# Performance work log

Measured on AMD Instinct MI355X. Metric: run time of the kernel, lower is better.

The kernel has to match this reference:

```python
import jax, jax.numpy as jnp
import numpy as np

DN = ('NCHW', 'OIHW', 'NCHW')

def conv(x, w, b, stride=1, pad=1):
    y = jax.lax.conv_general_dilated(x, w, (stride, stride), [(pad, pad), (pad, pad)], dimension_numbers=DN)
    return y + b[None, :, None, None]

def conv_t(x, w, b):
    # torch ConvTranspose2d(k=4, s=2, p=1): implemented as lhs-dilated conv, pad = k-1-p = 2
    y = jax.lax.conv_general_dilated(x, w, (1, 1), [(2, 2), (2, 2)], lhs_dilation=(2, 2), dimension_numbers=DN)
    return y + b[None, :, None, None]

def residual_stack(x, rw3, rb3, rw1, rb1):
    # canonical VQ-VAE residual block: x + conv1x1(relu(conv3x3(relu(x)))), then final relu
    n = rw3.shape[0]
    for i in range(n):
        h = conv(jax.nn.relu(x), rw3[i], rb3[i], 1, 1)
        h = conv(jax.nn.relu(h), rw1[i], rb1[i], 1, 0)
        x = x + h
    return jax.nn.relu(x)

def vq(x, codebook, beta):
    # x: [N, D, H, W] -> [N, H, W, D]
    x = jnp.transpose(x, (0, 2, 3, 1))
    shp = x.shape
    xf = x.reshape(-1, shp[-1])                               # [T, D]
    d = (jnp.sum(xf * xf, 1, keepdims=True)
         + jnp.sum(codebook * codebook, 1)
         - 2.0 * xf @ codebook.T)                             # [T, K]
    idx = jnp.argmin(d, axis=1)                               # [T]
    enc = jax.nn.one_hot(idx, codebook.shape[0], dtype=x.dtype)
    q = jnp.take(codebook, idx, axis=0).reshape(shp)
    loss_e = jnp.mean((jax.lax.stop_gradient(q) - x) ** 2)
    loss_q = jnp.mean((q - jax.lax.stop_gradient(x)) ** 2)
    loss = loss_q + beta * loss_e
    q_st = x + jax.lax.stop_gradient(q - x)
    p = jnp.mean(enc, axis=0)
    perplexity = jnp.exp(-jnp.sum(p * jnp.log(p + 1e-10)))
    return loss, jnp.transpose(q_st, (0, 3, 1, 2)), perplexity, enc

def setup_inputs() -> dict:
    key = jax.random.key(0)
    ks = jax.random.split(key, 24)
    C_img, C, RH, NR, K, D = 3, 128, 32, 2, 512, 64
    def g(k, shape, fan_in):
        return jax.random.normal(k, shape, jnp.float32) * (1.0 / np.sqrt(fan_in))
    inp = {
        'x': jax.random.normal(ks[0], (16, C_img, 256, 256), jnp.float32),
        'enc_w1': g(ks[1], (C // 2, C_img, 4, 4), C_img * 16), 'enc_b1': jnp.zeros((C // 2,)),
        'enc_w2': g(ks[2], (C, C // 2, 4, 4), C // 2 * 16), 'enc_b2': jnp.zeros((C,)),
        'enc_w3': g(ks[3], (C, C, 3, 3), C * 9), 'enc_b3': jnp.zeros((C,)),
        'enc_rw3': g(ks[4], (NR, RH, C, 3, 3), C * 9), 'enc_rb3': jnp.zeros((NR, RH)),
        'enc_rw1': g(ks[5], (NR, C, RH, 1, 1), RH), 'enc_rb1': jnp.zeros((NR, C)),
        'pre_w': g(ks[6], (D, C, 1, 1), C), 'pre_b': jnp.zeros((D,)),
        'codebook': jax.random.uniform(ks[7], (K, D), jnp.float32, -1.0 / K, 1.0 / K),
        'dec_w1': g(ks[8], (C, D, 3, 3), D * 9), 'dec_b1': jnp.zeros((C,)),
        'dec_rw3': g(ks[9], (NR, RH, C, 3, 3), C * 9), 'dec_rb3': jnp.zeros((NR, RH)),
        'dec_rw1': g(ks[10], (NR, C, RH, 1, 1), RH), 'dec_rb1': jnp.zeros((NR, C)),
        'dec_dw1': g(ks[11], (C // 2, C, 4, 4), C * 16), 'dec_db1': jnp.zeros((C // 2,)),
        'dec_dw2': g(ks[12], (C_img, C // 2, 4, 4), C // 2 * 16), 'dec_db2': jnp.zeros((C_img,)),
    }
    return inp

def reference(x, enc_w1, enc_b1, enc_w2, enc_b2, enc_w3, enc_b3, enc_rw3, enc_rb3, enc_rw1, enc_rb1,
              pre_w, pre_b, codebook, dec_w1, dec_b1, dec_rw3, dec_rb3, dec_rw1, dec_rb1,
              dec_dw1, dec_db1, dec_dw2, dec_db2):
    beta = 0.25
    # encoder
    h = jax.nn.relu(conv(x, enc_w1, enc_b1, 2, 1))
    h = jax.nn.relu(conv(h, enc_w2, enc_b2, 2, 1))
    h = conv(h, enc_w3, enc_b3, 1, 1)
    h = residual_stack(h, enc_rw3, enc_rb3, enc_rw1, enc_rb1)
    # pre-VQ 1x1 conv
    z = conv(h, pre_w, pre_b, 1, 0)
    # vector quantization
    loss, q, perplexity, _ = vq(z, codebook, beta)
    # decoder
    d = conv(q, dec_w1, dec_b1, 1, 1)
    d = residual_stack(d, dec_rw3, dec_rb3, dec_rw1, dec_rb1)
    d = jax.nn.relu(conv_t(d, dec_dw1, dec_db1))
    x_recon = conv_t(d, dec_dw2, dec_db2)
    return loss, x_recon, perplexity
```

## Files before the change

### kernel.cpp

```cpp
#include <hip/hip_runtime.h>

typedef __attribute__((ext_vector_type(8)))  short bf16x8;
typedef __attribute__((ext_vector_type(16))) float f32x16;
typedef unsigned long long u64t;

__device__ __forceinline__ int swzu(int u)
{
    return u ^ (((u >> 3) & 1) | (((u >> 4) & 1) << 1));
}

__device__ __forceinline__ void fsplit(float v, unsigned short& h, unsigned short& l)
{
    union { float f; unsigned u; } a; a.f = v;
    unsigned uh = a.u + 0x7fffu + ((a.u >> 16) & 1u);
    h = (unsigned short)(uh >> 16);
    union { float f; unsigned u; } hb; hb.u = (unsigned)h << 16;
    float r = v - hb.f;
    union { float f; unsigned u; } b; b.f = r;
    unsigned ul = b.u + 0x7fffu + ((b.u >> 16) & 1u);
    l = (unsigned short)(ul >> 16);
}

__device__ __forceinline__ float bf2f(unsigned short u)
{
    union { float f; unsigned v; } a; a.v = (unsigned)u << 16; return a.f;
}

__global__ void pack_w(const float* __restrict__ w, unsigned short* __restrict__ hi,
                       unsigned short* __restrict__ lo, int Cout, int Cin, int KK,
                       int CoP, int CiP)
{
    int i = blockIdx.x * 256 + threadIdx.x;
    int tot = KK * CoP * CiP;
    if (i >= tot) return;
    int t  = i / (CoP * CiP);
    int r  = i - t * (CoP * CiP);
    int co = r / CiP;
    int ci = r - co * CiP;
    float v = (co < Cout && ci < Cin) ? w[((size_t)co * Cin + ci) * KK + t] : 0.f;
    unsigned short h, l;
    fsplit(v, h, l);
    hi[i] = h; lo[i] = l;
}

__global__ void cb_norm(const float* __restrict__ cb, float* __restrict__ cn)
{
    int i = blockIdx.x * 256 + threadIdx.x;
    if (i >= 512) return;
    float s = 0.f;
    for (int d = 0; d < 64; d++) s = fmaf(cb[i*64+d], cb[i*64+d], s);
    cn[i] = s;
}

__global__ __launch_bounds__(256) void pack_x(const float* __restrict__ x,
    unsigned short* __restrict__ PH)
{
    int idx = blockIdx.x * 256 + threadIdx.x;
    int n = idx >> 16, pix = idx & 65535;
    unsigned short h[8], l[8];
#pragma unroll
    for (int c = 0; c < 8; c++) h[c] = 0;
#pragma unroll
    for (int c = 0; c < 3; c++) {
        float v = x[((size_t)(n * 3 + c) << 16) + pix];
        fsplit(v, h[c], l[c]);
    }
    uint4 hv;
    hv.x = h[0] | ((unsigned)h[1] << 16); hv.y = h[2] | ((unsigned)h[3] << 16);
    hv.z = h[4] | ((unsigned)h[5] << 16); hv.w = h[6] | ((unsigned)h[7] << 16);
    uint4 z4 = make_uint4(0, 0, 0, 0);
    size_t b0 = (((size_t)(n * 2) << 16) + pix) * 8;
    size_t b1 = (((size_t)(n * 2 + 1) << 16) + pix) * 8;
    *(uint4*)(PH + b0) = hv;
    *(uint4*)(PH + b1) = z4;
}

template<int K,int S,int P,int CIP,int COUT,int HIN,int WIN,int HOUT,int WOUT,
         int TR,int TC,int WM,int WN,int PX2,int CO2,int CC,int CO_PAD,
         bool PACK,bool PRELU,bool PLO,bool WF32,bool ROUT,bool RES>
__global__ __launch_bounds__(256) void conv_mfma(
    const unsigned short* __restrict__ inH,
    const unsigned short* __restrict__ wpH,
    const float* __restrict__ bias, const float* __restrict__ res,
    float* __restrict__ outF, unsigned short* __restrict__ outPH,
    unsigned short* __restrict__ outPL)
{
    constexpr int IHT = (TR - 1) * S + K;
    constexpr int IW  = (TC - 1) * S + K;
    constexpr int PS  = IHT * IW;
    constexpr int PLN = CC * 2;
    constexpr int UN  = PS * PLN;
    constexpr int KK  = K * K;
    constexpr int NCH = CIP / (CC * 16);
    constexpr int NBUF = (NCH > 1) ? 2 : 1;
    constexpr int CG  = CIP / 8;
    constexpr int CGO = (COUT + 7) / 8;
    constexpr int XB  = WOUT / TC;
    constexpr int REGU = (UN + 255) / 256;
    constexpr int NST = CC * KK;

    __shared__ uint4 lbH[NBUF * UN];

    const int tid = threadIdx.x;
    const int bx  = blockIdx.x;
    const int r0  = (bx / XB) * TR;
    const int c0  = (bx % XB) * TC;
    const int co0 = blockIdx.y * (WM * CO2 * 32);
    const int n   = blockIdx.z;

    const int l  = tid & 63, wv = tid >> 6;
    const int wm = wv / WN, wn = wv % WN;
    const int ln = l & 31, kg = l >> 5;

    int pb[PX2], gyv[PX2], gxv[PX2];
#pragma unroll
    for (int p2 = 0; p2 < PX2; p2++) {
        int q = wn * (PX2 * 32) + p2 * 32 + ln;
        int lr = q / TC, lc = q % TC;
        pb[p2] = (lr * S) * IW + lc * S;
        gyv[p2] = r0 + lr; gxv[p2] = c0 + lc;
    }

    const int iy0 = r0 * S - P, ix0 = c0 * S - P;
    const size_t inb = (size_t)n * CG * HIN * WIN;

    f32x16 acc[PX2][CO2];
#pragma unroll
    for (int p2 = 0; p2 < PX2; p2++)
#pragma unroll
        for (int g = 0; g < CO2; g++) acc[p2][g] = (f32x16){};

    auto unit_load = [&](int u, int cgb, uint4& hv){
        int kgu = u / PS, pos = u - kgu * PS;
        int py = pos / IW, px = pos - py * IW;
        int gy = iy0 + py, gx = ix0 + px;
        bool ok = ((unsigned)gy < (unsigned)HIN) && ((unsigned)gx < (unsigned)WIN);
        hv = make_uint4(0,0,0,0);
        if (ok) {
            size_t a = (inb + ((size_t)(cgb + kgu) * HIN + gy) * WIN + gx) * 8;
            hv = *(const uint4*)(inH + a);
        }
    };

    auto stage_direct = [&](int kc, int b){
        for (int idx = tid; idx < UN; idx += 256) {
            uint4 hv;
            unit_load(idx, kc * PLN, hv);
            lbH[b * UN + swzu(idx)] = hv;
        }
    };

    uint4 rvH[REGU];
    auto load_regs = [&](int kc){
#pragma unroll
        for (int rr = 0; rr < REGU; rr++) {
            int idx = tid + rr * 256;
            uint4 hv = make_uint4(0,0,0,0);
            if (idx < UN) unit_load(idx, kc * PLN, hv);
            rvH[rr] = hv;
        }
    };
    auto write_regs = [&](int b){
#pragma unroll
        for (int rr = 0; rr < REGU; rr++) {
            int idx = tid + rr * 256;
            if (idx < UN) lbH[b * UN + swzu(idx)] = rvH[rr];
        }
    };

    auto compute = [&](int kc, int b){
        bf16x8 aR[4][CO2], bR[3][PX2];
        auto loadA = [&](int step, bf16x8 (&a)[CO2]){
            const int ks = step / KK, t = step - ks * KK;
#pragma unroll
            for (int g = 0; g < CO2; g++) {
                const int coA = co0 + (wm * CO2 + g) * 32 + ln;
                const size_t wo = ((size_t)t * CO_PAD + coA) * CIP
                                + kc * (CC * 16) + ks * 16 + kg * 8;
                a[g] = *(const bf16x8*)(wpH + wo);
            }
        };
        auto loadB = [&](int step, bf16x8 (&bv)[PX2]){
            const int ks = step / KK, t = step - ks * KK;
            const int ky = t / K, kx = t - ky * K;
#pragma unroll
            for (int p2 = 0; p2 < PX2; p2++) {
                const int u = (ks * 2 + kg) * PS + pb[p2] + ky * IW + kx;
                bv[p2] = *(const bf16x8*)&lbH[b * UN + swzu(u)];
            }
        };
        loadA(0, aR[0]);
        if (NST > 1) loadA(1, aR[1]);
        if (NST > 2) loadA(2, aR[2]);
        loadB(0, bR[0]);
        if (NST > 1) loadB(1, bR[1]);
        __builtin_amdgcn_s_setprio(1);
#pragma unroll
        for (int step = 0; step < NST; step++) {
            if (step + 3 < NST) loadA(step + 3, aR[(step + 3) & 3]);
            if (step + 2 < NST) loadB(step + 2, bR[(step + 2) % 3]);
#pragma unroll
            for (int p2 = 0; p2 < PX2; p2++)
#pragma unroll
                for (int g = 0; g < CO2; g++)
                    acc[p2][g] = __builtin_amdgcn_mfma_f32_32x32x16_bf16(
                        aR[step & 3][g], bR[step % 3][p2], acc[p2][g], 0, 0, 0);
        }
        __builtin_amdgcn_s_setprio(0);
    };

    stage_direct(0, 0);
    __syncthreads();
    int cur = 0;
    for (int kc = 0; kc < NCH; kc++) {
        const bool more = (kc + 1 < NCH);
        if (more) load_regs(kc + 1);
        compute(kc, cur);
        if (more) {
            write_regs(cur ^ 1);
            __syncthreads();
            cur ^= 1;
        }
    }

    const size_t HWo = (size_t)HOUT * WOUT;
#pragma unroll
    for (int p2 = 0; p2 < PX2; p2++) {
        const int gy = gyv[p2], gx = gxv[p2];
#pragma unroll
        for (int g = 0; g < CO2; g++) {
            const int co32 = co0 + (wm * CO2 + g) * 32;
#pragma unroll
            for (int rq = 0; rq < 4; rq++) {
                const int cb4 = co32 + 8 * rq + 4 * kg;
                float v[4];
#pragma unroll
                for (int i = 0; i < 4; i++) {
                    const int r = rq * 4 + i;
                    const int co = cb4 + i;
                    float bv = (co < COUT) ? bias[co] : 0.f;
                    float vv = acc[p2][g][r] + bv;
                    if (RES && co < COUT)
                        vv += res[((size_t)n * COUT + co) * HWo + (size_t)gy * WOUT + gx];
                    if (ROUT) vv = fmaxf(vv, 0.f);
                    if (WF32 && co < COUT)
                        outF[((size_t)n * COUT + co) * HWo + (size_t)gy * WOUT + gx] = vv;
                    v[i] = vv;
                }
                if (PACK) {
                    u64t uh = 0, ul = 0;
#pragma unroll
                    for (int i = 0; i < 4; i++) {
                        float pv = PRELU ? fmaxf(v[i], 0.f) : v[i];
                        unsigned short ph, pl;
                        fsplit(pv, ph, pl);
                        uh |= (u64t)ph << (16 * i);
                        ul |= (u64t)pl << (16 * i);
                    }
                    size_t pa = (((size_t)n * CGO + (co32 >> 3) + rq) * HOUT + gy) * (size_t)WOUT * 8
                              + (size_t)gx * 8 + 4 * kg;
                    *(u64t*)(outPH + pa) = uh;
                    if (PLO) *(u64t*)(outPL + pa) = ul;
                }
            }
        }
    }
}

template<int CIP,int COUT,int HW,int CO_PAD,
         bool PACK,bool PRELU,bool PLO,bool WF32,bool ROUT,bool RES>
__global__ __launch_bounds__(256) void conv1x1_mfma(
    const unsigned short* __restrict__ inH,
    const unsigned short* __restrict__ wpH,
    const float* __restrict__ bias, const float* __restrict__ res,
    float* __restrict__ outF, unsigned short* __restrict__ outPH,
    unsigned short* __restrict__ outPL)
{
    constexpr int NCH = CIP / 16;
    constexpr int CG  = CIP / 8;
    constexpr int CGO = (COUT + 7) / 8;

    const int tid = threadIdx.x;
    const int bx  = blockIdx.x;
    const int co0 = blockIdx.y * 64;
    const int n   = blockIdx.z;

    const int l  = tid & 63, wv = tid >> 6;
    const int wm = wv >> 1, wn = wv & 1;
    const int ln = l & 31, kg = l >> 5;

    const int pix = bx * 64 + wn * 32 + ln;
    const int coA = co0 + wm * 32 + ln;

    f32x16 acc = {};
#pragma unroll
    for (int kc = 0; kc < NCH; kc++) {
        bf16x8 b = *(const bf16x8*)(inH + ((size_t)(n * CG + kc * 2 + kg) * HW + pix) * 8);
        bf16x8 a = *(const bf16x8*)(wpH + ((size_t)coA * CIP + kc * 16 + kg * 8));
        acc = __builtin_amdgcn_mfma_f32_32x32x16_bf16(a, b, acc, 0, 0, 0);
    }

    const int co32 = co0 + wm * 32;
#pragma unroll
    for (int rq = 0; rq < 4; rq++) {
        const int cb4 = co32 + 8 * rq + 4 * kg;
        float v[4];
#pragma unroll
        for (int i = 0; i < 4; i++) {
            const int r = rq * 4 + i;
            const int co = cb4 + i;
            float bv = (co < COUT) ? bias[co] : 0.f;
            float vv = acc[r] + bv;
            if (RES && co < COUT)
                vv += res[((size_t)n * COUT + co) * HW + pix];
            if (ROUT) vv = fmaxf(vv, 0.f);
            if (WF32 && co < COUT)
                outF[((size_t)n * COUT + co) * HW + pix] = vv;
            v[i] = vv;
        }
        if (PACK) {
            u64t uh = 0, ul = 0;
#pragma unroll
            for (int i = 0; i < 4; i++) {
                float pv = PRELU ? fmaxf(v[i], 0.f) : v[i];
                unsigned short ph, pl;
                fsplit(pv, ph, pl);
                uh |= (u64t)ph << (16 * i);
                ul |= (u64t)pl << (16 * i);
            }
            size_t pa = (((size_t)n * CGO + (co32 >> 3) + rq) * HW + pix) * 8 + 4 * kg;
            *(u64t*)(outPH + pa) = uh;
            if (PLO) *(u64t*)(outPL + pa) = ul;
        }
    }
}

template<int CIP,int COUT,int HIN,int WIN,int CO2,int CC,int CO_PAD,
         bool PACK,bool WF32,bool ROUT>
__global__ __launch_bounds__(256) void convt_mfma(
    const unsigned short* __restrict__ inH,
    const unsigned short* __restrict__ wpH,
    const float* __restrict__ bias, float* __restrict__ outF,
    unsigned short* __restrict__ outPH)
{
    constexpr int HOUT = 2 * HIN, WOUT = 2 * WIN;
    constexpr int XHN  = WOUT / 128;
    constexpr int PS   = 3 * 68;
    constexpr int PLN  = CC * 2;
    constexpr int UN   = PS * PLN;
    constexpr int NCH  = CIP / (CC * 16);
    constexpr int NBUF = (NCH > 1) ? 2 : 1;
    constexpr int CG   = CIP / 8;
    constexpr int CGO  = (COUT + 7) / 8;
    constexpr int REGU = (UN + 255) / 256;
    constexpr int NST  = CC * 4;

    __shared__ uint4 lbH[NBUF * UN];

    const int tid = threadIdx.x;
    const int xh  = blockIdx.x % XHN;
    const int gr  = blockIdx.x / XHN;
    const int oy0 = (gr >> 1) * 4 + (gr & 1);
    const int co0 = blockIdx.y * (CO2 * 32);
    const int n   = blockIdx.z;

    const int ky0 = oy0 & 1;
    const int iyb = ((oy0 + ky0) >> 1) - 1;

    const int l  = tid & 63, wv = tid >> 6;
    const int pw = wv & 1, xb = wv >> 1;
    const int ln = l & 31, kg = l >> 5;

    const size_t inb = (size_t)n * CG * HIN * WIN;

    f32x16 acc[2][CO2];
#pragma unroll
    for (int r2 = 0; r2 < 2; r2++)
#pragma unroll
        for (int g = 0; g < CO2; g++) acc[r2][g] = (f32x16){};

    auto unit_load = [&](int u, int cgb, uint4& hv){
        int kgu = u / PS, pos = u - kgu * PS;
        int rr = pos / 68, cc = pos - rr * 68;
        int gy = iyb + rr, gx = xh * 64 + cc - 1;
        bool ok = ((unsigned)gy < (unsigned)HIN) && ((unsigned)gx < (unsigned)WIN);
        hv = make_uint4(0,0,0,0);
        if (ok) {
            size_t a = (inb + ((size_t)(cgb + kgu) * HIN + gy) * WIN + gx) * 8;
            hv = *(const uint4*)(inH + a);
        }
    };

    auto stage_direct = [&](int kc, int b){
        for (int idx = tid; idx < UN; idx += 256) {
            uint4 hv;
            unit_load(idx, kc * PLN, hv);
            lbH[b * UN + swzu(idx)] = hv;
        }
    };

    uint4 rvH[REGU];
    auto load_regs = [&](int kc){
#pragma unroll
        for (int rr = 0; rr < REGU; rr++) {
            int idx = tid + rr * 256;
            uint4 hv = make_uint4(0,0,0,0);
            if (idx < UN) unit_load(idx, kc * PLN, hv);
            rvH[rr] = hv;
        }
    };
    auto write_regs = [&](int b){
#pragma unroll
        for (int rr = 0; rr < REGU; rr++) {
            int idx = tid + rr * 256;
            if (idx < UN) lbH[b * UN + swzu(idx)] = rvH[rr];
        }
    };

    auto compute = [&](int kc, int b){
        bf16x8 aR[4][CO2], bR[3][2];
        auto loadA = [&](int step, bf16x8 (&a)[CO2]){
            const int ks = step / 4, tt = step - ks * 4;
            const int widx = (ky0 + 2 * (tt >> 1)) * 4 + (pw + 2 * (tt & 1));
#pragma unroll
            for (int g = 0; g < CO2; g++) {
                const int coA = co0 + g * 32 + ln;
                const size_t wo = ((size_t)widx * CO_PAD + coA) * CIP
                                + kc * (CC * 16) + ks * 16 + kg * 8;
                a[g] = *(const bf16x8*)(wpH + wo);
            }
        };
        auto loadB = [&](int step, bf16x8 (&bv)[2]){
            const int ks = step / 4, tt = step - ks * 4;
            const int ty = tt >> 1, tx = tt & 1;
#pragma unroll
            for (int r2 = 0; r2 < 2; r2++) {
                const int u = (ks * 2 + kg) * PS + (r2 + ty) * 68 + xb * 32 + ln + pw + tx;
                bv[r2] = *(const bf16x8*)&lbH[b * UN + swzu(u)];
            }
        };
        loadA(0, aR[0]);
        if (NST > 1) loadA(1, aR[1]);
        if (NST > 2) loadA(2, aR[2]);
        loadB(0, bR[0]);
        if (NST > 1) loadB(1, bR[1]);
        __builtin_amdgcn_s_setprio(1);
#pragma unroll
        for (int step = 0; step < NST; step++) {
            if (step + 3 < NST) loadA(step + 3, aR[(step + 3) & 3]);
            if (step + 2 < NST) loadB(step + 2, bR[(step + 2) % 3]);
#pragma unroll
            for (int r2 = 0; r2 < 2; r2++)
#pragma unroll
                for (int g = 0; g < CO2; g++)
                    acc[r2][g] = __builtin_amdgcn_mfma_f32_32x32x16_bf16(
                        aR[step & 3][g], bR[step % 3][r2], acc[r2][g], 0, 0, 0);
        }
        __builtin_amdgcn_s_setprio(0);
    };

    stage_direct(0, 0);
    __syncthreads();
    int cur = 0;
    for (int kc = 0; kc < NCH; kc++) {
        const bool more = (kc + 1 < NCH);
        if (more) load_regs(kc + 1);
        compute(kc, cur);
        if (more) {
            write_regs(cur ^ 1);
            __syncthreads();
            cur ^= 1;
        }
    }

    const int ox = xh * 128 + pw + 2 * (xb * 32 + ln);
    const size_t HWo = (size_t)HOUT * WOUT;
#pragma unroll
    for (int r2 = 0; r2 < 2; r2++) {
        const int oy = oy0 + 2 * r2;
#pragma unroll
        for (int g = 0; g < CO2; g++) {
            const int co32 = co0 + g * 32;
#pragma unroll
            for (int rq = 0; rq < 4; rq++) {
                const int cb4 = co32 + 8 * rq + 4 * kg;
                float v[4];
#pragma unroll
                for (int i = 0; i < 4; i++) {
                    const int r = rq * 4 + i;
                    const int co = cb4 + i;
                    float bv = (co < COUT) ? bias[co] : 0.f;
                    float vv = acc[r2][g][r] + bv;
                    if (ROUT) vv = fmaxf(vv, 0.f);
                    if (WF32 && co < COUT)
                        outF[((size_t)n * COUT + co) * HWo + (size_t)oy * WOUT + ox] = vv;
                    v[i] = vv;
                }
                if (PACK) {
                    u64t uh = 0;
#pragma unroll
                    for (int i = 0; i < 4; i++) {
                        unsigned short ph, pl;
                        fsplit(v[i], ph, pl);
                        uh |= (u64t)ph << (16 * i);
                    }
                    size_t pa = (((size_t)n * CGO + (co32 >> 3) + rq) * HOUT + oy) * (size_t)WOUT * 8
                              + (size_t)ox * 8 + 4 * kg;
                    *(u64t*)(outPH + pa) = uh;
                }
            }
        }
    }
}

__global__ __launch_bounds__(256) void vq_mfma(
    const unsigned short* __restrict__ zPH, const unsigned short* __restrict__ zPL,
    const unsigned short* __restrict__ cbH, const unsigned short* __restrict__ cbL,
    const float* __restrict__ cnorm,
    unsigned short* __restrict__ qPH,
    float* __restrict__ ssep, int* __restrict__ hist)
{
    __shared__ unsigned short zH[128 * 72];
    __shared__ unsigned short zL[128 * 72];
    __shared__ float cnl[512];
    __shared__ int   hl[512];

    const int tid = threadIdx.x;
    const int blk = blockIdx.x;

    for (int i = tid; i < 512; i += 256) { cnl[i] = cnorm[i]; hl[i] = 0; }

    for (int idx = tid; idx < 1024; idx += 256) {
        int tok = idx >> 3, cg = idx & 7;
        int t = blk * 128 + tok;
        int n = t >> 12, pix = t & 4095;
        size_t a = (((size_t)(n * 8 + cg)) * 4096 + pix) * 8;
        *(uint4*)&zH[tok * 72 + cg * 8] = *(const uint4*)(zPH + a);
        *(uint4*)&zL[tok * 72 + cg * 8] = *(const uint4*)(zPL + a);
    }
    __syncthreads();

    const int l  = tid & 63, wv = tid >> 6;
    const int ln = l & 31, kg = l >> 5;
    const int tok = wv * 32 + ln;

    float xn = 0.f;
#pragma unroll
    for (int j8 = 0; j8 < 8; j8++) {
        bf16x8 vH = *(const bf16x8*)&zH[tok * 72 + j8 * 8];
        bf16x8 vL = *(const bf16x8*)&zL[tok * 72 + j8 * 8];
#pragma unroll
        for (int j = 0; j < 8; j++) {
            float xv = bf2f((unsigned short)vH[j]) + bf2f((unsigned short)vL[j]);
            xn = fmaf(xv, xv, xn);
        }
    }

    float bm = 3.4e38f; int bidx = 0;
    for (int cg = 0; cg < 16; cg++) {
        f32x16 a0 = {}, a1 = {};
#pragma unroll
        for (int ks = 0; ks < 4; ks++) {
            const size_t wo = ((size_t)(cg * 32 + ln)) * 64 + ks * 16 + kg * 8;
            bf16x8 aH = *(const bf16x8*)(cbH + wo);
            bf16x8 aL = *(const bf16x8*)(cbL + wo);
            bf16x8 bH = *(const bf16x8*)&zH[tok * 72 + ks * 16 + kg * 8];
            bf16x8 bL = *(const bf16x8*)&zL[tok * 72 + ks * 16 + kg * 8];
            a0 = __builtin_amdgcn_mfma_f32_32x32x16_bf16(aH, bH, a0, 0, 0, 0);
            a1 = __builtin_amdgcn_mfma_f32_32x32x16_bf16(aH, bL, a1, 0, 0, 0);
            a1 = __builtin_amdgcn_mfma_f32_32x32x16_bf16(aL, bH, a1, 0, 0, 0);
        }
#pragma unroll
        for (int r = 0; r < 16; r++) {
            int m    = (r & 3) + 8 * (r >> 2) + 4 * kg;
            int code = cg * 32 + m;
            float s  = a0[r] + a1[r];
            float dm = cnl[code] - 2.f * s;
            if (dm < bm) { bm = dm; bidx = code; }
        }
    }

    float bm2 = __shfl_xor(bm, 32);
    int   bi2 = __shfl_xor(bidx, 32);
    if (bm2 < bm || (bm2 == bm && bi2 < bidx)) { bm = bm2; bidx = bi2; }

    {
        int t = blk * 128 + tok;
        int n = t >> 12, pix = t & 4095;
#pragma unroll
        for (int cgl = 0; cgl < 4; cgl++) {
            int cg = kg * 4 + cgl;
            uint4 hv = *(const uint4*)(cbH + (size_t)bidx * 64 + cg * 8);
            size_t a = (((size_t)(n * 8 + cg)) * 4096 + pix) * 8;
            *(uint4*)(qPH + a) = hv;
        }
    }

    float bestd = xn + bm;
    float c = (kg == 0) ? bestd : 0.f;
#pragma unroll
    for (int o = 32; o > 0; o >>= 1) c += __shfl_down(c, o, 64);
    if (l == 0) ssep[blk * 4 + wv] = c;
    if (kg == 0) atomicAdd(&hl[bidx], 1);
    __syncthreads();
    for (int i = tid; i < 512; i += 256) if (hl[i] > 0) atomicAdd(&hist[i], hl[i]);
}

__global__ void vq_init(int* hist)
{
    for (int i = threadIdx.x; i < 512; i += 256) hist[i] = 0;
}

__global__ __launch_bounds__(256) void vq_finalize(
    const float* __restrict__ ssep, const int* __restrict__ hist,
    float* __restrict__ o_loss, float* __restrict__ o_perp)
{
    __shared__ float red[256];
    const int tid = threadIdx.x;
    float h = 0.f;
    for (int i = tid; i < 512; i += 256) {
        float p = (float)hist[i] * (1.0f / 65536.0f);
        h -= p * logf(p + 1e-10f);
    }
    red[tid] = h;
    __syncthreads();
    for (int st = 128; st > 0; st >>= 1) {
        if (tid < st) red[tid] += red[tid + st];
        __syncthreads();
    }
    const float H = red[0];
    __syncthreads();
    float s = 0.f;
    for (int i = tid; i < 2048; i += 256) s += ssep[i];
    red[tid] = s;
    __syncthreads();
    for (int st = 128; st > 0; st >>= 1) {
        if (tid < st) red[tid] += red[tid + st];
        __syncthreads();
    }
    if (tid == 0) {
        *o_loss = 1.25f * red[0] / 4194304.0f;
        *o_perp = expf(H);
    }
}

extern "C" void kernel_launch(void* const* d_in, const int* in_sizes, int n_in,
                              void* d_out, int out_size, void* d_ws, size_t ws_size,
                              hipStream_t stream)
{
    const float* x       = (const float*)d_in[0];
    const float* enc_w1  = (const float*)d_in[1];
    const float* enc_b1  = (const float*)d_in[2];
    const float* enc_w2  = (const float*)d_in[3];
    const float* enc_b2  = (const float*)d_in[4];
    const float* enc_w3  = (const float*)d_in[5];
    const float* enc_b3  = (const float*)d_in[6];
    const float* enc_rw3 = (const float*)d_in[7];
    const float* enc_rb3 = (const float*)d_in[8];
    const float* enc_rw1 = (const float*)d_in[9];
    const float* enc_rb1 = (const float*)d_in[10];
    const float* pre_w   = (const float*)d_in[11];
    const float* pre_b   = (const float*)d_in[12];
    const float* cb      = (const float*)d_in[13];
    const float* dec_w1  = (const float*)d_in[14];
    const float* dec_b1  = (const float*)d_in[15];
    const float* dec_rw3 = (const float*)d_in[16];
    const float* dec_rb3 = (const float*)d_in[17];
    const float* dec_rw1 = (const float*)d_in[18];
    const float* dec_rb1 = (const float*)d_in[19];
    const float* dw1     = (const float*)d_in[20];
    const float* db1     = (const float*)d_in[21];
    const float* dw2     = (const float*)d_in[22];
    const float* db2     = (const float*)d_in[23];

    float* o      = (float*)d_out;
    float* loss_p = o;
    float* recon  = o + 1;
    float* perp_p = o + 1 + 16 * 3 * 256 * 256;

    unsigned short* R1H = (unsigned short*)d_ws;
    unsigned short* R1L = R1H + 16777216;
    unsigned short* R2H = R1L + 16777216;
    unsigned short* R2L = R2H + 16777216;
    float* Cf  = (float*)(R2L + 16777216);
    float* SSE = Cf + 8388608;
    int*   HIST = (int*)(SSE + 2048);

    unsigned short *xPH = R1H;
    unsigned short *BPH = R1H;
    unsigned short *zPH = R1H + 8388608, *zPL = R1L + 8388608;
    unsigned short *DtPH = R1H + 12582912;
    unsigned short *dAPH = R1H;
    unsigned short *APH = R2H;
    unsigned short *CPH = R2H;
    unsigned short *qPH = R2H + 8388608;

    unsigned short* wp_cur = (unsigned short*)(((size_t)(HIST + 512) + 31) & ~(size_t)31);
    auto carve = [&](size_t n_us) {
        unsigned short* p = wp_cur;
        wp_cur += ((n_us + 15) & ~(size_t)15);
        return p;
    };
    auto PK = [&](const float* w, unsigned short* hi, unsigned short* lo,
                  int Co, int Ci, int KK, int CoP, int CiP) {
        int tot = KK * CoP * CiP;
        pack_w<<<dim3((tot + 255) / 256), dim3(256), 0, stream>>>(w, hi, lo, Co, Ci, KK, CoP, CiP);
    };

    unsigned short *e1H = carve(16*64*16),  *e1L = carve(16*64*16);
    unsigned short *e2H = carve(16*128*64), *e2L = carve(16*128*64);
    unsigned short *e3H = carve(9*128*128), *e3L = carve(9*128*128);
    unsigned short *er3aH = carve(9*32*128), *er3aL = carve(9*32*128);
    unsigned short *er3bH = carve(9*32*128), *er3bL = carve(9*32*128);
    unsigned short *er1aH = carve(128*32),   *er1aL = carve(128*32);
    unsigned short *er1bH = carve(128*32),   *er1bL = carve(128*32);
    unsigned short *preH = carve(64*128),    *preL = carve(64*128);
    unsigned short *d1H  = carve(9*128*64),  *d1L  = carve(9*128*64);
    unsigned short *dr3aH = carve(9*32*128), *dr3aL = carve(9*32*128);
    unsigned short *dr3bH = carve(9*32*128), *dr3bL = carve(9*32*128);
    unsigned short *dr1aH = carve(128*32),   *dr1aL = carve(128*32);
    unsigned short *dr1bH = carve(128*32),   *dr1bL = carve(128*32);
    unsigned short *ct1H = carve(16*64*128), *ct1L = carve(16*64*128);
    unsigned short *ct2H = carve(16*32*64),  *ct2L = carve(16*32*64);
    unsigned short *cbH  = carve(512*64),    *cbL  = carve(512*64);
    float* CN = (float*)carve(1024);

    PK(enc_w1, e1H, e1L, 64, 3, 16, 64, 16);
    PK(enc_w2, e2H, e2L, 128, 64, 16, 128, 64);
    PK(enc_w3, e3H, e3L, 128, 128, 9, 128, 128);
    PK(enc_rw3,             er3aH, er3aL, 32, 128, 9, 32, 128);
    PK(enc_rw3 + 32*128*9,  er3bH, er3bL, 32, 128, 9, 32, 128);
    PK(enc_rw1,             er1aH, er1aL, 128, 32, 1, 128, 32);
    PK(enc_rw1 + 128*32,    er1bH, er1bL, 128, 32, 1, 128, 32);
    PK(pre_w, preH, preL, 64, 128, 1, 64, 128);
    PK(dec_w1, d1H, d1L, 128, 64, 9, 128, 64);
    PK(dec_rw3,             dr3aH, dr3aL, 32, 128, 9, 32, 128);
    PK(dec_rw3 + 32*128*9,  dr3bH, dr3bL, 32, 128, 9, 32, 128);
    PK(dec_rw1,             dr1aH, dr1aL, 128, 32, 1, 128, 32);
    PK(dec_rw1 + 128*32,    dr1bH, dr1bL, 128, 32, 1, 128, 32);
    PK(dw1, ct1H, ct1L, 64, 128, 16, 64, 128);
    PK(dw2, ct2H, ct2L, 3, 64, 16, 32, 64);
    PK(cb,  cbH,  cbL,  512, 64, 1, 512, 64);
    cb_norm<<<dim3(2), dim3(256), 0, stream>>>(cb, CN);
    pack_x<<<dim3(4096), dim3(256), 0, stream>>>(x, xPH);

    const int N = 16;

    conv_mfma<4,2,1, 16,64, 256,256, 128,128, 2,64, 2,2,2,1, 1, 64,
              true,false,false,false,true,false>
        <<<dim3(128,1,N),256,0,stream>>>(xPH, e1H, enc_b1, nullptr, nullptr, APH, nullptr);
    conv_mfma<4,2,1, 64,128, 128,128, 64,64, 2,64, 2,2,2,2, 1, 128,
              true,false,false,false,true,false>
        <<<dim3(32,1,N),256,0,stream>>>(APH, e2H, enc_b2, nullptr, nullptr, BPH, nullptr);
    conv_mfma<3,1,1, 128,128, 64,64, 64,64, 2,64, 2,2,2,2, 2, 128,
              true,true,false,true,false,false>
        <<<dim3(32,1,N),256,0,stream>>>(BPH, e3H, enc_b3, nullptr, Cf, CPH, nullptr);
    conv_mfma<3,1,1, 128,32, 64,64, 64,64, 2,64, 1,4,1,1, 2, 32,
              true,true,false,false,false,false>
        <<<dim3(32,1,N),256,0,stream>>>(CPH, er3aH, enc_rb3, nullptr, nullptr, DtPH, nullptr);
    conv1x1_mfma<32,128, 4096, 128,  true,true,false,true,false,true>
        <<<dim3(64,2,N),256,0,stream>>>(DtPH, er1aH, enc_rb1, Cf, Cf, CPH, nullptr);
    conv_mfma<3,1,1, 128,32, 64,64, 64,64, 2,64, 1,4,1,1, 2, 32,
              true,true,false,false,false,false>
        <<<dim3(32,1,N),256,0,stream>>>(CPH, er3bH, enc_rb3 + 32, nullptr, nullptr, DtPH, nullptr);
    conv1x1_mfma<32,128, 4096, 128,  true,true,false,true,false,true>
        <<<dim3(64,2,N),256,0,stream>>>(DtPH, er1bH, enc_rb1 + 128, Cf, Cf, CPH, nullptr);
    conv1x1_mfma<128,64, 4096, 64,   true,false,true,false,false,false>
        <<<dim3(64,1,N),256,0,stream>>>(CPH, preH, pre_b, nullptr, nullptr, zPH, zPL);

    vq_init<<<dim3(1), dim3(256), 0, stream>>>(HIST);
    vq_mfma<<<dim3(512), dim3(256), 0, stream>>>(zPH, zPL, cbH, cbL, CN, qPH, SSE, HIST);
    vq_finalize<<<dim3(1), dim3(256), 0, stream>>>(SSE, HIST, loss_p, perp_p);

    conv_mfma<3,1,1, 64,128, 64,64, 64,64, 2,64, 2,2,2,2, 2, 128,
              true,true,false,true,false,false>
        <<<dim3(32,1,N),256,0,stream>>>(qPH, d1H, dec_b1, nullptr, Cf, CPH, nullptr);
    conv_mfma<3,1,1, 128,32, 64,64, 64,64, 2,64, 1,4,1,1, 2, 32,
              true,true,false,false,false,false>
        <<<dim3(32,1,N),256,0,stream>>>(CPH, dr3aH, dec_rb3, nullptr, nullptr, DtPH, nullptr);
    conv1x1_mfma<32,128, 4096, 128,  true,true,false,true,false,true>
        <<<dim3(64,2,N),256,0,stream>>>(DtPH, dr1aH, dec_rb1, Cf, Cf, CPH, nullptr);
    conv_mfma<3,1,1, 128,32, 64,64, 64,64, 2,64, 1,4,1,1, 2, 32,
              true,true,false,false,false,false>
        <<<dim3(32,1,N),256,0,stream>>>(CPH, dr3bH, dec_rb3 + 32, nullptr, nullptr, DtPH, nullptr);
    conv1x1_mfma<32,128, 4096, 128,  true,true,false,true,false,true>
        <<<dim3(64,2,N),256,0,stream>>>(DtPH, dr1bH, dec_rb1 + 128, Cf, Cf, CPH, nullptr);
    convt_mfma<128,64, 64,64, 2, 2, 64,  true,false,true>
        <<<dim3(64,1,N),256,0,stream>>>(CPH, ct1H, db1, nullptr, dAPH);
    convt_mfma<64,3, 128,128, 1, 2, 32,  false,true,false>
        <<<dim3(256,1,N),256,0,stream>>>(dAPH, ct2H, db2, recon, nullptr);
}
```

Measured before the change: 533.6 us.

## Preload all A-fragments per chunk and split output channels across grid y

The conv and transposed-conv compute loops now load every weight fragment for the whole K-chunk into registers up front, replacing the rolling 4-deep prefetch ring. Three 128-output-channel convs drop one CO2 template parameter from 2 to 1 and double grid.y, so each block covers half the output channels. Together these cut per-thread register pressure from accumulators and double the number of blocks in flight. In exchange the input tile staged in shared memory is now loaded twice, once per channel half, and the larger upfront weight array may raise VGPR use for the larger NST shapes.

```diff
diff --git a/kernel.cpp b/kernel.cpp
--- a/kernel.cpp
+++ b/kernel.cpp
@@ -169,17 +169,19 @@
     };
 
     auto compute = [&](int kc, int b){
-        bf16x8 aR[4][CO2], bR[3][PX2];
-        auto loadA = [&](int step, bf16x8 (&a)[CO2]){
-            const int ks = step / KK, t = step - ks * KK;
+        bf16x8 aF[NST * CO2];
+#pragma unroll
+        for (int s2 = 0; s2 < NST; s2++) {
+            const int ks = s2 / KK, t = s2 - ks * KK;
 #pragma unroll
             for (int g = 0; g < CO2; g++) {
                 const int coA = co0 + (wm * CO2 + g) * 32 + ln;
                 const size_t wo = ((size_t)t * CO_PAD + coA) * CIP
                                 + kc * (CC * 16) + ks * 16 + kg * 8;
-                a[g] = *(const bf16x8*)(wpH + wo);
+                aF[s2 * CO2 + g] = *(const bf16x8*)(wpH + wo);
             }
-        };
+        }
+        bf16x8 bR[3][PX2];
         auto loadB = [&](int step, bf16x8 (&bv)[PX2]){
             const int ks = step / KK, t = step - ks * KK;
             const int ky = t / K, kx = t - ky * K;
@@ -189,22 +191,18 @@
                 bv[p2] = *(const bf16x8*)&lbH[b * UN + swzu(u)];
             }
         };
-        loadA(0, aR[0]);
-        if (NST > 1) loadA(1, aR[1]);
-        if (NST > 2) loadA(2, aR[2]);
         loadB(0, bR[0]);
         if (NST > 1) loadB(1, bR[1]);
         __builtin_amdgcn_s_setprio(1);
 #pragma unroll
         for (int step = 0; step < NST; step++) {
-            if (step + 3 < NST) loadA(step + 3, aR[(step + 3) & 3]);
             if (step + 2 < NST) loadB(step + 2, bR[(step + 2) % 3]);
 #pragma unroll
             for (int p2 = 0; p2 < PX2; p2++)
 #pragma unroll
                 for (int g = 0; g < CO2; g++)
                     acc[p2][g] = __builtin_amdgcn_mfma_f32_32x32x16_bf16(
-                        aR[step & 3][g], bR[step % 3][p2], acc[p2][g], 0, 0, 0);
+                        aF[step * CO2 + g], bR[step % 3][p2], acc[p2][g], 0, 0, 0);
         }
         __builtin_amdgcn_s_setprio(0);
     };
@@ -418,18 +416,20 @@
     };
 
     auto compute = [&](int kc, int b){
-        bf16x8 aR[4][CO2], bR[3][2];
-        auto loadA = [&](int step, bf16x8 (&a)[CO2]){
-            const int ks = step / 4, tt = step - ks * 4;
+        bf16x8 aF[NST * CO2];
+#pragma unroll
+        for (int s2 = 0; s2 < NST; s2++) {
+            const int ks = s2 / 4, tt = s2 - ks * 4;
             const int widx = (ky0 + 2 * (tt >> 1)) * 4 + (pw + 2 * (tt & 1));
 #pragma unroll
             for (int g = 0; g < CO2; g++) {
                 const int coA = co0 + g * 32 + ln;
                 const size_t wo = ((size_t)widx * CO_PAD + coA) * CIP
                                 + kc * (CC * 16) + ks * 16 + kg * 8;
-                a[g] = *(const bf16x8*)(wpH + wo);
+                aF[s2 * CO2 + g] = *(const bf16x8*)(wpH + wo);
             }
-        };
+        }
+        bf16x8 bR[3][2];
         auto loadB = [&](int step, bf16x8 (&bv)[2]){
             const int ks = step / 4, tt = step - ks * 4;
             const int ty = tt >> 1, tx = tt & 1;
@@ -439,22 +439,18 @@
                 bv[r2] = *(const bf16x8*)&lbH[b * UN + swzu(u)];
             }
         };
-        loadA(0, aR[0]);
-        if (NST > 1) loadA(1, aR[1]);
-        if (NST > 2) loadA(2, aR[2]);
         loadB(0, bR[0]);
         if (NST > 1) loadB(1, bR[1]);
         __builtin_amdgcn_s_setprio(1);
 #pragma unroll
         for (int step = 0; step < NST; step++) {
-            if (step + 3 < NST) loadA(step + 3, aR[(step + 3) & 3]);
             if (step + 2 < NST) loadB(step + 2, bR[(step + 2) % 3]);
 #pragma unroll
             for (int r2 = 0; r2 < 2; r2++)
 #pragma unroll
                 for (int g = 0; g < CO2; g++)
                     acc[r2][g] = __builtin_amdgcn_mfma_f32_32x32x16_bf16(
-                        aR[step & 3][g], bR[step % 3][r2], acc[r2][g], 0, 0, 0);
+                        aF[step * CO2 + g], bR[step % 3][r2], acc[r2][g], 0, 0, 0);
         }
         __builtin_amdgcn_s_setprio(0);
     };
@@ -749,12 +745,12 @@
     conv_mfma<4,2,1, 16,64, 256,256, 128,128, 2,64, 2,2,2,1, 1, 64,
               true,false,false,false,true,false>
         <<<dim3(128,1,N),256,0,stream>>>(xPH, e1H, enc_b1, nullptr, nullptr, APH, nullptr);
-    conv_mfma<4,2,1, 64,128, 128,128, 64,64, 2,64, 2,2,2,2, 1, 128,
+    conv_mfma<4,2,1, 64,128, 128,128, 64,64, 2,64, 2,2,2,1, 1, 128,
               true,false,false,false,true,false>
-        <<<dim3(32,1,N),256,0,stream>>>(APH, e2H, enc_b2, nullptr, nullptr, BPH, nullptr);
-    conv_mfma<3,1,1, 128,128, 64,64, 64,64, 2,64, 2,2,2,2, 2, 128,
+        <<<dim3(32,2,N),256,0,stream>>>(APH, e2H, enc_b2, nullptr, nullptr, BPH, nullptr);
+    conv_mfma<3,1,1, 128,128, 64,64, 64,64, 2,64, 2,2,2,1, 2, 128,
               true,true,false,true,false,false>
-        <<<dim3(32,1,N),256,0,stream>>>(BPH, e3H, enc_b3, nullptr, Cf, CPH, nullptr);
+        <<<dim3(32,2,N),256,0,stream>>>(BPH, e3H, enc_b3, nullptr, Cf, CPH, nullptr);
     conv_mfma<3,1,1, 128,32, 64,64, 64,64, 2,64, 1,4,1,1, 2, 32,
               true,true,false,false,false,false>
         <<<dim3(32,1,N),256,0,stream>>>(CPH, er3aH, enc_rb3, nullptr, nullptr, DtPH, nullptr);
@@ -772,9 +768,9 @@
     vq_mfma<<<dim3(512), dim3(256), 0, stream>>>(zPH, zPL, cbH, cbL, CN, qPH, SSE, HIST);
     vq_finalize<<<dim3(1), dim3(256), 0, stream>>>(SSE, HIST, loss_p, perp_p);
 
-    conv_mfma<3,1,1, 64,128, 64,64, 64,64, 2,64, 2,2,2,2, 2, 128,
+    conv_mfma<3,1,1, 64,128, 64,64, 64,64, 2,64, 2,2,2,1, 2, 128,
               true,true,false,true,false,false>
-        <<<dim3(32,1,N),256,0,stream>>>(qPH, d1H, dec_b1, nullptr, Cf, CPH, nullptr);
+        <<<dim3(32,2,N),256,0,stream>>>(qPH, d1H, dec_b1, nullptr, Cf, CPH, nullptr);
     conv_mfma<3,1,1, 128,32, 64,64, 64,64, 2,64, 1,4,1,1, 2, 32,
               true,true,false,false,false,false>
         <<<dim3(32,1,N),256,0,stream>>>(CPH, dr3aH, dec_rb3, nullptr, nullptr, DtPH, nullptr);
```

Result: slower. 550.1 us (+3.1%).
